# Performance work log

Measured on AMD Instinct MI355X. Metric: run time of the kernel, lower is better.

The kernel has to match this reference:

```python
import jax, jax.numpy as jnp
from jax import lax
import numpy as np

NUM_HEAD = 12
EPS = 1e-5            # torch LayerNorm default
NEG_INF = 1.0e12      # self.inf_value in the source
LEAKY_SLOPE = 0.01    # torch LeakyReLU default
MASK_FIRST = True     # maskedAtten=True applies only to block 0


def _layer_norm(x, s, b):
    m = jnp.mean(x, axis=-1, keepdims=True)
    v = jnp.var(x, axis=-1, keepdims=True)
    return (x - m) / jnp.sqrt(v + EPS) * s + b


def _forward(x, conv_w, conv_b, pos, ln0_s, ln0_b, Wq, bq, Wk, bk, Wv, bv,
             Wo, bo, ln1_s, ln1_b, W1, b1, W2, b2, proj_w, proj_b):
    B, C, H, W = x.shape
    E = conv_w.shape[0]
    P = conv_w.shape[-1]
    hd = E // NUM_HEAD

    # patch embed: Conv2d(C, E, P, stride=P)
    h = lax.conv_general_dilated(x, conv_w, (P, P), 'VALID',
                                 dimension_numbers=('NCHW', 'OIHW', 'NCHW'))
    h = h + conv_b[None, :, None, None]
    L = h.shape[2] * h.shape[3]
    h = h.reshape(B, E, L).transpose(0, 2, 1) + pos  # (B, L, E)

    causal = jnp.triu(jnp.ones((L, L), dtype=bool), 1)
    n_layers = Wq.shape[0]
    for i in range(n_layers):
        # --- attention block ---
        xn = _layer_norm(h, ln0_s[i], ln0_b[i])
        q = (xn @ Wq[i] + bq[i]).reshape(B, L, NUM_HEAD, hd).transpose(0, 2, 1, 3)
        k = (xn @ Wk[i] + bk[i]).reshape(B, L, NUM_HEAD, hd).transpose(0, 2, 1, 3)
        v = (xn @ Wv[i] + bv[i]).reshape(B, L, NUM_HEAD, hd).transpose(0, 2, 1, 3)
        scores = jnp.einsum('bhqd,bhkd->bhqk', q, k) * (hd ** -0.5)
        if i == 0 and MASK_FIRST:
            scores = jnp.where(causal, -NEG_INF, scores)
        a = jax.nn.softmax(scores, axis=-1)
        o = jnp.einsum('bhqk,bhkd->bhqd', a, v)  # (B, NH, L, hd)
        # faithful to torch source: reshape(bs, l, emb) WITHOUT permuting heads back
        o = o.reshape(B, L, E)
        o = o @ Wo[i] + bo[i]
        h = o + h  # residual onto pre-LN input
        # --- MLP block ---
        xr = _layer_norm(h, ln1_s[i], ln1_b[i])
        m = xr @ W1[i] + b1[i]
        m = jnp.where(m >= 0, m, LEAKY_SLOPE * m)
        m = m @ W2[i] + b2[i]
        h = m + xr  # residual onto post-LN (as in source)

    y = h @ proj_w + proj_b               # (B, L, C*P*P)
    y = y.transpose(0, 2, 1).reshape(B, C, H, W)
    return y


def setup_inputs() -> dict:
    key = jax.random.key(0)
    B, C, H, W = 8, 3, 384, 384
    P, E, NL = 16, 768, 8
    FF = 4 * E
    L = (H // P) * (W // P)  # 576
    CPP = C * P * P          # 768
    s = 0.02
    ks = jax.random.split(key, 24)
    f32 = jnp.float32
    inp = {
        'x': jax.random.normal(ks[0], (B, C, H, W), f32),
        'conv_w': jax.random.normal(ks[1], (E, C, P, P), f32) * s,
        'conv_b': jax.random.normal(ks[2], (E,), f32) * s,
        'pos': jax.random.normal(ks[3], (1, L, E), f32),
        'ln0_s': jnp.ones((NL, E), f32),
        'ln0_b': jnp.zeros((NL, E), f32),
        'Wq': jax.random.normal(ks[4], (NL, E, E), f32) * s,
        'bq': jax.random.normal(ks[5], (NL, E), f32) * s,
        'Wk': jax.random.normal(ks[6], (NL, E, E), f32) * s,
        'bk': jax.random.normal(ks[7], (NL, E), f32) * s,
        'Wv': jax.random.normal(ks[8], (NL, E, E), f32) * s,
        'bv': jax.random.normal(ks[9], (NL, E), f32) * s,
        'Wo': jax.random.normal(ks[10], (NL, E, E), f32) * s,
        'bo': jax.random.normal(ks[11], (NL, E), f32) * s,
        'ln1_s': jnp.ones((NL, E), f32),
        'ln1_b': jnp.zeros((NL, E), f32),
        'W1': jax.random.normal(ks[12], (NL, E, FF), f32) * s,
        'b1': jax.random.normal(ks[13], (NL, FF), f32) * s,
        'W2': jax.random.normal(ks[14], (NL, FF, E), f32) * s,
        'b2': jax.random.normal(ks[15], (NL, E), f32) * s,
        'proj_w': jax.random.normal(ks[16], (E, CPP), f32) * s,
        'proj_b': jax.random.normal(ks[17], (CPP,), f32) * s,
    }
    return inp


def reference(x, conv_w, conv_b, pos, ln0_s, ln0_b, Wq, bq, Wk, bk, Wv, bv,
              Wo, bo, ln1_s, ln1_b, W1, b1, W2, b2, proj_w, proj_b):
    return _forward(x, conv_w, conv_b, pos, ln0_s, ln0_b, Wq, bq, Wk, bk,
                    Wv, bv, Wo, bo, ln1_s, ln1_b, W1, b1, W2, b2,
                    proj_w, proj_b)
```

## Files before the change

kernel.cpp:

```cpp
#include <hip/hip_runtime.h>
#include <hip/hip_bf16.h>
#include <stdint.h>

#define NLAYERS 8
#define LSEQ 576
#define EMB 768
#define NHEAD 12
#define HDIM 64
#define FFDIM 3072
#define BLROWS 4608

typedef __attribute__((ext_vector_type(8))) short short8;
typedef __attribute__((ext_vector_type(4))) float floatx4;

__device__ __forceinline__ float b2f(short s) {
    union { float f; uint32_t u; } x; x.u = ((uint32_t)(uint16_t)s) << 16; return x.f;
}
__device__ __forceinline__ short f2b(float f) {
    union { float f; uint32_t u; } x; x.f = f;
    uint32_t r = x.u + 0x7fffu + ((x.u >> 16) & 1u);
    return (short)(r >> 16);
}

#define GLDS16(gp, lp) __builtin_amdgcn_global_load_lds( \
    (const __attribute__((address_space(1))) void*)(gp), \
    (__attribute__((address_space(3))) void*)(lp), 16, 0, 0)

__device__ __forceinline__ void xcd_remap(int& bx, int& by) {
    const int gx = gridDim.x;
    const int n  = gx * gridDim.y;
    const int orig = by * gx + bx;
    const int q = n >> 3, r = n & 7;
    const int xcd = orig & 7;
    const int wgid = (xcd < r ? xcd * (q + 1) : r * (q + 1) + (xcd - r) * q) + (orig >> 3);
    bx = wgid % gx;
    by = wgid / gx;
}

template<int DEPTH, int RES, bool ADD_POS, bool LEAKY, int OUTM, bool QKV>
__global__ __launch_bounds__(256)
void gemm_bt(const short* __restrict__ A, const short* __restrict__ Bt,
             const float* __restrict__ bias, const float* __restrict__ pos,
             const void* __restrict__ res, void* __restrict__ Cout,
             short* __restrict__ aux_kp, short* __restrict__ aux_vt,
             int N, int K)
{
    __shared__ short As[DEPTH * 64 * 64];
    __shared__ short Bs[DEPTH * 128 * 64];
    int bx = blockIdx.x, by = blockIdx.y;
    xcd_remap(bx, by);
    const int t    = threadIdx.x;
    const int lane = t & 63;
    const int w    = t >> 6;
    const int m0   = by * 64;
    const int n0   = bx * 128;
    const int wm   = (w >> 1) * 32;
    const int wn   = (w & 1) * 64;

    floatx4 acc[2][4];
#pragma unroll
    for (int i = 0; i < 2; ++i)
#pragma unroll
        for (int j = 0; j < 4; ++j)
            acc[i][j] = (floatx4){0.f, 0.f, 0.f, 0.f};

    const int srow = t >> 3;
    const int sch  = t & 7;
    const short* Ag = A  + (size_t)m0 * K;
    const short* Bg = Bt + (size_t)n0 * K;
    const int nt = K >> 6;

#define STAGE(buf, k0)                                                              \
    {                                                                               \
        _Pragma("unroll")                                                           \
        for (int i = 0; i < 2; ++i) {                                               \
            int row = srow + i * 32;                                                \
            GLDS16(Ag + (size_t)row * K + (k0) + ((sch ^ (row & 7)) << 3),          \
                   &As[(buf) * 4096 + (size_t)(t + i * 256) * 8]);                  \
        }                                                                           \
        _Pragma("unroll")                                                           \
        for (int i = 0; i < 4; ++i) {                                               \
            int row = srow + i * 32;                                                \
            GLDS16(Bg + (size_t)row * K + (k0) + ((sch ^ (row & 7)) << 3),          \
                   &Bs[(buf) * 8192 + (size_t)(t + i * 256) * 8]);                  \
        }                                                                           \
    }

#define COMPUTE(buf)                                                                \
    {                                                                               \
        _Pragma("unroll")                                                           \
        for (int ks = 0; ks < 2; ++ks) {                                            \
            short8 af[2], bf[4];                                                    \
            _Pragma("unroll")                                                       \
            for (int i = 0; i < 2; ++i) {                                           \
                int row = wm + i * 16 + (lane & 15);                                \
                int ch  = (ks * 4 + (lane >> 4)) ^ (row & 7);                       \
                af[i] = *(const short8*)&As[(buf) * 4096 + row * 64 + ch * 8];      \
            }                                                                       \
            _Pragma("unroll")                                                       \
            for (int j = 0; j < 4; ++j) {                                           \
                int row = wn + j * 16 + (lane & 15);                                \
                int ch  = (ks * 4 + (lane >> 4)) ^ (row & 7);                       \
                bf[j] = *(const short8*)&Bs[(buf) * 8192 + row * 64 + ch * 8];      \
            }                                                                       \
            _Pragma("unroll")                                                       \
            for (int i = 0; i < 2; ++i)                                             \
                _Pragma("unroll")                                                   \
                for (int j = 0; j < 4; ++j)                                         \
                    acc[i][j] = __builtin_amdgcn_mfma_f32_16x16x32_bf16(            \
                        af[i], bf[j], acc[i][j], 0, 0, 0);                          \
        }                                                                           \
    }

    if constexpr (DEPTH == 2) {
        STAGE(0, 0);
        __syncthreads();
        int cur = 0;
        for (int k0 = 0; k0 < K; k0 += 64) {
            if (k0 + 64 < K) STAGE(cur ^ 1, k0 + 64);
            COMPUTE(cur);
            __syncthreads();
            cur ^= 1;
        }
    } else {
        STAGE(0, 0);
        STAGE(1, 64);
        asm volatile("s_waitcnt vmcnt(6)" ::: "memory");
        __builtin_amdgcn_sched_barrier(0);
        __builtin_amdgcn_s_barrier();
        int cur = 0, stg = 2;
        for (int tt = 0; tt < nt; ++tt) {
            if (tt + 2 < nt) STAGE(stg, (tt + 2) << 6);
            COMPUTE(cur);
            if (tt + 1 < nt) {
                if (tt + 2 < nt) { asm volatile("s_waitcnt vmcnt(6)" ::: "memory"); }
                else             { asm volatile("s_waitcnt vmcnt(0)" ::: "memory"); }
                __builtin_amdgcn_sched_barrier(0);
                __builtin_amdgcn_s_barrier();
                __builtin_amdgcn_sched_barrier(0);
            }
            cur = (cur + 1 == DEPTH) ? 0 : cur + 1;
            stg = (stg + 1 == DEPTH) ? 0 : stg + 1;
        }
    }
#undef STAGE
#undef COMPUTE

    const int colb = n0 + wn + (lane & 15);
    const int rowb = m0 + wm + ((lane >> 4) * 4);
#pragma unroll
    for (int i = 0; i < 2; ++i) {
#pragma unroll
        for (int j = 0; j < 4; ++j) {
            const int col = colb + j * 16;
            const float bv = bias[col];
#pragma unroll
            for (int r = 0; r < 4; ++r) {
                const int row = rowb + i * 16 + r;
                float v = acc[i][j][r] + bv;
                if constexpr (ADD_POS) v += pos[(size_t)(row % LSEQ) * N + col];
                if constexpr (RES == 1) v += ((const float*)res)[(size_t)row * N + col];
                if constexpr (RES == 2) v += b2f(((const short*)res)[(size_t)row * N + col]);
                if constexpr (LEAKY)   v = v >= 0.f ? v : 0.01f * v;
                if constexpr (QKV) {
                    const int b = row / LSEQ, l = row % LSEQ;
                    const short sv16 = f2b(v);
                    if (col < 768) {
                        ((short*)Cout)[(size_t)row * 768 + col] = sv16;
                    } else if (col < 1536) {
                        const int d = col - 768, hh = d >> 6, dd = d & 63;
                        const size_t bh = (size_t)b * 12 + hh;
                        aux_kp[(bh * LSEQ + l) * 64 + (dd & 7) + (((dd >> 3) ^ (l & 7)) << 3)] = sv16;
                    } else {
                        const int d = col - 1536, hh = d >> 6, dd = d & 63;
                        const size_t bh = (size_t)b * 12 + hh;
                        aux_vt[(bh * 64 + dd) * LSEQ + (l & ~63) + ((l & 63) ^ ((dd & 7) << 3))] = sv16;
                    }
                } else if constexpr (OUTM == 1) {
                    ((float*)Cout)[(size_t)row * N + col] = v;
                } else if constexpr (OUTM == 2) {
                    ((float*)Cout)[(size_t)row * N + col] = v;
                    aux_kp[(size_t)row * N + col] = f2b(v);
                } else {
                    ((short*)Cout)[(size_t)row * N + col] = f2b(v);
                }
            }
        }
    }
}

__global__ __launch_bounds__(256)
void ln_kernel(const float* __restrict__ h, const float* __restrict__ g,
               const float* __restrict__ bbias, short* __restrict__ outb)
{
    const int row = blockIdx.x;
    const float* x = h + (size_t)row * EMB;
    const int t = threadIdx.x;
    float v0 = x[t], v1 = x[t + 256], v2 = x[t + 512];
    float s  = v0 + v1 + v2;
    float ss = v0 * v0 + v1 * v1 + v2 * v2;
#pragma unroll
    for (int m = 1; m < 64; m <<= 1) {
        s  += __shfl_xor(s, m, 64);
        ss += __shfl_xor(ss, m, 64);
    }
    __shared__ float red[8];
    if ((t & 63) == 0) { red[t >> 6] = s; red[4 + (t >> 6)] = ss; }
    __syncthreads();
    float S  = red[0] + red[1] + red[2] + red[3];
    float SS = red[4] + red[5] + red[6] + red[7];
    float mean = S * (1.f / 768.f);
    float var  = SS * (1.f / 768.f) - mean * mean;
    float rstd = rsqrtf(var + 1e-5f);
    const size_t base = (size_t)row * EMB;
#pragma unroll
    for (int q = 0; q < 3; ++q) {
        int e = t + q * 256;
        float v = (q == 0 ? v0 : (q == 1 ? v1 : v2));
        float y = (v - mean) * rstd * g[e] + bbias[e];
        outb[base + e] = f2b(y);
    }
}

__global__ __launch_bounds__(256)
void attn_mfma(const short* __restrict__ qbuf, const short* __restrict__ kp,
               const short* __restrict__ vt, short* __restrict__ oout, int causal)
{
    const int qt = blockIdx.x, bh = blockIdx.y;
    const int b = bh / 12, h = bh % 12;
    const int t = threadIdx.x, lane = t & 63, w = t >> 6;

    __shared__ short Ks[64 * 64];
    __shared__ short Vs[64 * 64];
    __shared__ short Plds[4][16][72];

    const int nrow = lane & 15;
    const int kch  = (lane >> 4) * 8;
    const int swz  = (lane & 7) << 3;

    short8 aq[2];
    {
        const short* qrow = qbuf + ((size_t)(b * LSEQ) + qt * 64 + w * 16 + nrow) * 768 + h * 64 + kch;
        aq[0] = *(const short8*)qrow;
        aq[1] = *(const short8*)(qrow + 32);
    }

    float m[4], lsum[4];
    floatx4 oacc[4];
#pragma unroll
    for (int r = 0; r < 4; ++r) { m[r] = -3e38f; lsum[r] = 0.f; }
#pragma unroll
    for (int j = 0; j < 4; ++j) oacc[j] = (floatx4){0.f, 0.f, 0.f, 0.f};

    const int ktend = causal ? qt : 8;
    const short* ksrc = kp + ((size_t)bh * LSEQ) * 64;
    const short* vsrc = vt + ((size_t)bh * 64) * LSEQ;

    for (int kt = 0; kt <= ktend; ++kt) {
        __syncthreads();
        {
            const short* kt_src = ksrc + (size_t)(kt * 64) * 64;
            GLDS16(kt_src + (size_t)t * 8,          &Ks[(size_t)t * 8]);
            GLDS16(kt_src + (size_t)(t + 256) * 8,  &Ks[(size_t)(t + 256) * 8]);
            int f0 = t, f1 = t + 256;
            GLDS16(vsrc + (size_t)(f0 >> 3) * LSEQ + kt * 64 + (f0 & 7) * 8, &Vs[(size_t)f0 * 8]);
            GLDS16(vsrc + (size_t)(f1 >> 3) * LSEQ + kt * 64 + (f1 & 7) * 8, &Vs[(size_t)f1 * 8]);
        }
        __syncthreads();

        floatx4 sc[4];
#pragma unroll
        for (int j = 0; j < 4; ++j) sc[j] = (floatx4){0.f, 0.f, 0.f, 0.f};
#pragma unroll
        for (int s = 0; s < 2; ++s) {
#pragma unroll
            for (int j = 0; j < 4; ++j) {
                short8 bk = *(const short8*)&Ks[(16 * j + nrow) * 64 + ((kch + 32 * s) ^ swz)];
                sc[j] = __builtin_amdgcn_mfma_f32_16x16x32_bf16(aq[s], bk, sc[j], 0, 0, 0);
            }
        }
        float sv[4][4];
#pragma unroll
        for (int j = 0; j < 4; ++j)
#pragma unroll
            for (int r = 0; r < 4; ++r) {
                float v = sc[j][r] * 0.125f;
                if (causal && kt == qt) {
                    int key = kt * 64 + 16 * j + nrow;
                    int qr  = qt * 64 + w * 16 + (lane >> 4) * 4 + r;
                    if (key > qr) v = -1e12f;
                }
                sv[j][r] = v;
            }
#pragma unroll
        for (int r = 0; r < 4; ++r) {
            float tm = fmaxf(fmaxf(sv[0][r], sv[1][r]), fmaxf(sv[2][r], sv[3][r]));
            tm = fmaxf(tm, __shfl_xor(tm, 1, 64));
            tm = fmaxf(tm, __shfl_xor(tm, 2, 64));
            tm = fmaxf(tm, __shfl_xor(tm, 4, 64));
            tm = fmaxf(tm, __shfl_xor(tm, 8, 64));
            float nm = fmaxf(m[r], tm);
            float c  = __expf(m[r] - nm);
            m[r] = nm;
            float ps = 0.f;
#pragma unroll
            for (int j = 0; j < 4; ++j) {
                float p = __expf(sv[j][r] - nm);
                sv[j][r] = p;
                ps += p;
            }
            lsum[r] = lsum[r] * c + ps;
#pragma unroll
            for (int j = 0; j < 4; ++j) oacc[j][r] *= c;
        }
#pragma unroll
        for (int j = 0; j < 4; ++j)
#pragma unroll
            for (int r = 0; r < 4; ++r)
                Plds[w][(lane >> 4) * 4 + r][16 * j + nrow] = f2b(sv[j][r]);
        short8 ap[2];
#pragma unroll
        for (int s = 0; s < 2; ++s)
            ap[s] = *(const short8*)&Plds[w][nrow][kch + 32 * s];
#pragma unroll
        for (int s = 0; s < 2; ++s) {
#pragma unroll
            for (int j = 0; j < 4; ++j) {
                short8 bv = *(const short8*)&Vs[(16 * j + nrow) * 64 + ((kch + 32 * s) ^ swz)];
                oacc[j] = __builtin_amdgcn_mfma_f32_16x16x32_bf16(ap[s], bv, oacc[j], 0, 0, 0);
            }
        }
    }

    float inv[4];
#pragma unroll
    for (int r = 0; r < 4; ++r) {
        float L = lsum[r];
        L += __shfl_xor(L, 1, 64);
        L += __shfl_xor(L, 2, 64);
        L += __shfl_xor(L, 4, 64);
        L += __shfl_xor(L, 8, 64);
        inv[r] = 1.f / L;
    }
#pragma unroll
    for (int j = 0; j < 4; ++j)
#pragma unroll
        for (int r = 0; r < 4; ++r) {
            size_t lq = (size_t)qt * 64 + w * 16 + (lane >> 4) * 4 + r;
            oout[((size_t)bh * LSEQ + lq) * 64 + 16 * j + nrow] = f2b(oacc[j][r] * inv[r]);
        }
}

__global__ void transpose_f2b(const float* __restrict__ in, short* __restrict__ out,
                              int R, int C, long long ibs, long long obs)
{
    __shared__ float tile[32][33];
    const int b = blockIdx.z;
    const float* inb = in + (long long)b * ibs;
    short* outb = out + (long long)b * obs;
    const int r0 = blockIdx.y * 32, c0 = blockIdx.x * 32;
    const int tx = threadIdx.x, ty = threadIdx.y;
#pragma unroll
    for (int i = 0; i < 32; i += 8) tile[ty + i][tx] = inb[(size_t)(r0 + ty + i) * C + c0 + tx];
    __syncthreads();
#pragma unroll
    for (int i = 0; i < 32; i += 8) outb[(size_t)(c0 + ty + i) * R + r0 + tx] = f2b(tile[tx][ty + i]);
}

__global__ void transpose_f2f(const float* __restrict__ in, float* __restrict__ out,
                              int R, int C, long long ibs, long long obs)
{
    __shared__ float tile[32][33];
    const int b = blockIdx.z;
    const float* inb = in + (long long)b * ibs;
    float* outb = out + (long long)b * obs;
    const int r0 = blockIdx.y * 32, c0 = blockIdx.x * 32;
    const int tx = threadIdx.x, ty = threadIdx.y;
#pragma unroll
    for (int i = 0; i < 32; i += 8) tile[ty + i][tx] = inb[(size_t)(r0 + ty + i) * C + c0 + tx];
    __syncthreads();
#pragma unroll
    for (int i = 0; i < 32; i += 8) outb[(size_t)(c0 + ty + i) * R + r0 + tx] = tile[tx][ty + i];
}

__global__ void concat_qkv_bias(const float* __restrict__ bq, const float* __restrict__ bk,
                                const float* __restrict__ bv, float* __restrict__ out)
{
    int i = blockIdx.x * 256 + threadIdx.x;
    int layer = i / 2304, j = i % 2304;
    float v;
    if (j < 768)       v = bq[layer * 768 + j];
    else if (j < 1536) v = bk[layer * 768 + j - 768];
    else               v = bv[layer * 768 + j - 1536];
    out[i] = v;
}

__global__ void im2col_kernel(const float* __restrict__ x, short* __restrict__ xcol)
{
    const size_t idx = (size_t)blockIdx.x * 256 + threadIdx.x;
    const int k = (int)(idx % 768);
    const size_t m = idx / 768;
    const int c  = k >> 8;
    const int ky = (k >> 4) & 15;
    const int kx = k & 15;
    const int b  = (int)(m / 576);
    const int l  = (int)(m % 576);
    const int ph = l / 24, pw = l % 24;
    xcol[idx] = f2b(x[((size_t)(b * 3 + c) * 384 + ph * 16 + ky) * 384 + pw * 16 + kx]);
}

__global__ void cast_f32_b16(const float* __restrict__ in, short* __restrict__ out, int n)
{
    int i = blockIdx.x * 256 + threadIdx.x;
    if (i < n) out[i] = f2b(in[i]);
}

extern "C" void kernel_launch(void* const* d_in, const int* in_sizes, int n_in,
                              void* d_out, int out_size, void* d_ws, size_t ws_size,
                              hipStream_t stream)
{
    const float* x      = (const float*)d_in[0];
    const float* conv_w = (const float*)d_in[1];
    const float* conv_b = (const float*)d_in[2];
    const float* pos    = (const float*)d_in[3];
    const float* ln0_s  = (const float*)d_in[4];
    const float* ln0_b  = (const float*)d_in[5];
    const float* Wq     = (const float*)d_in[6];
    const float* bq     = (const float*)d_in[7];
    const float* Wk     = (const float*)d_in[8];
    const float* bk     = (const float*)d_in[9];
    const float* Wv     = (const float*)d_in[10];
    const float* bv     = (const float*)d_in[11];
    const float* Wo     = (const float*)d_in[12];
    const float* bo     = (const float*)d_in[13];
    const float* ln1_s  = (const float*)d_in[14];
    const float* ln1_b  = (const float*)d_in[15];
    const float* W1     = (const float*)d_in[16];
    const float* b1     = (const float*)d_in[17];
    const float* W2     = (const float*)d_in[18];
    const float* b2     = (const float*)d_in[19];
    const float* proj_w = (const float*)d_in[20];
    const float* proj_b = (const float*)d_in[21];

    char* ws = (char*)d_ws;
    short* qkvT  = (short*)(ws);
    short* woT   = (short*)(ws + 28311552);
    short* w1T   = (short*)(ws + 37748736);
    short* w2T   = (short*)(ws + 75497472);
    short* projT = (short*)(ws + 113246208);
    float* qkvb  = (float*)(ws + 114425856);
    short* tmpA  = (short*)(ws + 114499584);
    float* h     = (float*)(ws + 142811136);
    short* xn    = (short*)(ws + 156966912);
    short* xrb   = (short*)(ws + 164044800);
    short* qbuf  = (short*)(ws + 185278464);
    short* o     = (short*)(ws + 206512128);
    short* convB = (short*)(ws + 213590016);

    short* kp = tmpA;
    short* vt = tmpA + 3538944;

    dim3 tb(32, 8);
    transpose_f2b<<<dim3(24, 24, 8), tb, 0, stream>>>(Wq, qkvT,           768, 768, 589824, 1769472);
    transpose_f2b<<<dim3(24, 24, 8), tb, 0, stream>>>(Wk, qkvT + 589824,  768, 768, 589824, 1769472);
    transpose_f2b<<<dim3(24, 24, 8), tb, 0, stream>>>(Wv, qkvT + 1179648, 768, 768, 589824, 1769472);
    transpose_f2b<<<dim3(24, 24, 8), tb, 0, stream>>>(Wo, woT,            768, 768, 589824, 589824);
    transpose_f2b<<<dim3(96, 24, 8), tb, 0, stream>>>(W1, w1T,            768, 3072, 2359296, 2359296);
    transpose_f2b<<<dim3(24, 96, 8), tb, 0, stream>>>(W2, w2T,            3072, 768, 2359296, 2359296);
    transpose_f2b<<<dim3(24, 24, 1), tb, 0, stream>>>(proj_w, projT,      768, 768, 0, 0);
    cast_f32_b16<<<2304, 256, 0, stream>>>(conv_w, convB, 589824);
    concat_qkv_bias<<<72, 256, 0, stream>>>(bq, bk, bv, qkvb);

    im2col_kernel<<<13824, 256, 0, stream>>>(x, tmpA);
    gemm_bt<3, 0, true, false, 1, false><<<dim3(6, 72), 256, 0, stream>>>(
        tmpA, convB, conv_b, pos, nullptr, h, nullptr, nullptr, 768, 768);

    for (int i = 0; i < NLAYERS; ++i) {
        ln_kernel<<<4608, 256, 0, stream>>>(h, ln0_s + i * 768, ln0_b + i * 768, xn);
        gemm_bt<2, 0, false, false, 0, true><<<dim3(18, 72), 256, 0, stream>>>(
            xn, qkvT + (size_t)i * 1769472, qkvb + i * 2304, nullptr, nullptr, qbuf, kp, vt, 2304, 768);
        attn_mfma<<<dim3(9, 96), 256, 0, stream>>>(qbuf, kp, vt, o, i == 0 ? 1 : 0);
        gemm_bt<3, 1, false, false, 1, false><<<dim3(6, 72), 256, 0, stream>>>(
            o, woT + (size_t)i * 589824, bo + i * 768, nullptr, h, h, nullptr, nullptr, 768, 768);
        ln_kernel<<<4608, 256, 0, stream>>>(h, ln1_s + i * 768, ln1_b + i * 768, xrb);
        gemm_bt<2, 0, false, true, 0, false><<<dim3(24, 72), 256, 0, stream>>>(
            xrb, w1T + (size_t)i * 2359296, b1 + i * 3072, nullptr, nullptr, tmpA, nullptr, nullptr, 3072, 768);
        if (i < NLAYERS - 1) {
            gemm_bt<3, 2, false, false, 1, false><<<dim3(6, 72), 256, 0, stream>>>(
                tmpA, w2T + (size_t)i * 2359296, b2 + i * 768, nullptr, xrb, h, nullptr, nullptr, 768, 3072);
        } else {
            gemm_bt<3, 2, false, false, 2, false><<<dim3(6, 72), 256, 0, stream>>>(
                tmpA, w2T + (size_t)i * 2359296, b2 + i * 768, nullptr, xrb, h, xn, nullptr, 768, 3072);
        }
    }

    short* hb = xn;
    float* yf = (float*)tmpA;
    gemm_bt<3, 0, false, false, 1, false><<<dim3(6, 72), 256, 0, stream>>>(
        hb, projT, proj_b, nullptr, nullptr, yf, nullptr, nullptr, 768, 768);
    transpose_f2f<<<dim3(24, 18, 8), tb, 0, stream>>>(yf, (float*)d_out, 576, 768, 442368, 442368);
}
```

Baseline: 1.620 ms.

## Split-K the N=768 GEMMs into two halves with a separate combine kernel

The GEMMs with N=768 (patch embed, out-projection, MLP down-projection, final projection) previously launched only 432 workgroups. They now split K across two z-slices, giving 864 workgroups. Each slice writes fp32 partials to its own buffer, and a new elementwise combine kernel adds the partials, bias, pos and residual, plus an optional bf16 copy. This is meant to fill the GPU's compute units better on these small-N GEMMs. The cost is an extra fp32 partial round-trip through memory and one more kernel launch per GEMM.

Result: slower. 1.780 ms (+9.9%).

```diff
diff --git a/kernel.cpp b/kernel.cpp
--- a/kernel.cpp
+++ b/kernel.cpp
@@ -11,6 +11,7 @@
 #define BLROWS 4608
 
 typedef __attribute__((ext_vector_type(8))) short short8;
+typedef __attribute__((ext_vector_type(4))) short short4v;
 typedef __attribute__((ext_vector_type(4))) float floatx4;
 
 __device__ __forceinline__ float b2f(short s) {
@@ -37,7 +38,7 @@
     by = wgid / gx;
 }
 
-template<int DEPTH, int RES, bool ADD_POS, bool LEAKY, int OUTM, bool QKV>
+template<int DEPTH, int RES, bool ADD_POS, bool LEAKY, int OUTM, bool QKV, bool SPLITK>
 __global__ __launch_bounds__(256)
 void gemm_bt(const short* __restrict__ A, const short* __restrict__ Bt,
              const float* __restrict__ bias, const float* __restrict__ pos,
@@ -57,6 +58,9 @@
     const int wm   = (w >> 1) * 32;
     const int wn   = (w & 1) * 64;
 
+    const int klen  = SPLITK ? (K >> 1) : K;
+    const int kbase = SPLITK ? blockIdx.z * klen : 0;
+
     floatx4 acc[2][4];
 #pragma unroll
     for (int i = 0; i < 2; ++i)
@@ -66,9 +70,9 @@
 
     const int srow = t >> 3;
     const int sch  = t & 7;
-    const short* Ag = A  + (size_t)m0 * K;
-    const short* Bg = Bt + (size_t)n0 * K;
-    const int nt = K >> 6;
+    const short* Ag = A  + (size_t)m0 * K + kbase;
+    const short* Bg = Bt + (size_t)n0 * K + kbase;
+    const int nt = klen >> 6;
 
 #define STAGE(buf, k0)                                                              \
     {                                                                               \
@@ -116,8 +120,8 @@
         STAGE(0, 0);
         __syncthreads();
         int cur = 0;
-        for (int k0 = 0; k0 < K; k0 += 64) {
-            if (k0 + 64 < K) STAGE(cur ^ 1, k0 + 64);
+        for (int k0 = 0; k0 < klen; k0 += 64) {
+            if (k0 + 64 < klen) STAGE(cur ^ 1, k0 + 64);
             COMPUTE(cur);
             __syncthreads();
             cur ^= 1;
@@ -148,6 +152,19 @@
 
     const int colb = n0 + wn + (lane & 15);
     const int rowb = m0 + wm + ((lane >> 4) * 4);
+
+    if constexpr (SPLITK) {
+        float* P = blockIdx.z ? (float*)aux_kp : (float*)Cout;
+#pragma unroll
+        for (int i = 0; i < 2; ++i)
+#pragma unroll
+            for (int j = 0; j < 4; ++j)
+#pragma unroll
+                for (int r = 0; r < 4; ++r)
+                    P[(size_t)(rowb + i * 16 + r) * N + colb + j * 16] = acc[i][j][r];
+        return;
+    }
+
 #pragma unroll
     for (int i = 0; i < 2; ++i) {
 #pragma unroll
@@ -189,6 +206,46 @@
     }
 }
 
+template<int RES, bool ADD_POS, int OUTM>
+__global__ __launch_bounds__(256)
+void combinek(const float* __restrict__ P0, const float* __restrict__ P1,
+              const float* __restrict__ bias, const float* __restrict__ pos,
+              const void* __restrict__ res, float* __restrict__ out,
+              short* __restrict__ auxb)
+{
+    const size_t i4 = ((size_t)blockIdx.x * 256 + threadIdx.x) * 4;
+    const int row = (int)(i4 / 768);
+    const int col = (int)(i4 % 768);
+    floatx4 a = *(const floatx4*)&P0[i4];
+    floatx4 b = *(const floatx4*)&P1[i4];
+    floatx4 bv = *(const floatx4*)&bias[col];
+    floatx4 v;
+#pragma unroll
+    for (int j = 0; j < 4; ++j) v[j] = a[j] + b[j] + bv[j];
+    if constexpr (ADD_POS) {
+        floatx4 p = *(const floatx4*)&pos[(size_t)(row % LSEQ) * 768 + col];
+#pragma unroll
+        for (int j = 0; j < 4; ++j) v[j] += p[j];
+    }
+    if constexpr (RES == 1) {
+        floatx4 rr = *(const floatx4*)&((const float*)res)[i4];
+#pragma unroll
+        for (int j = 0; j < 4; ++j) v[j] += rr[j];
+    }
+    if constexpr (RES == 2) {
+        short4v rr = *(const short4v*)&((const short*)res)[i4];
+#pragma unroll
+        for (int j = 0; j < 4; ++j) v[j] += b2f(rr[j]);
+    }
+    *(floatx4*)&out[i4] = v;
+    if constexpr (OUTM == 2) {
+        short4v ob;
+#pragma unroll
+        for (int j = 0; j < 4; ++j) ob[j] = f2b(v[j]);
+        *(short4v*)&auxb[i4] = ob;
+    }
+}
+
 __global__ __launch_bounds__(256)
 void ln_kernel(const float* __restrict__ h, const float* __restrict__ g,
                const float* __restrict__ bbias, short* __restrict__ outb)
@@ -459,6 +516,8 @@
 
     short* kp = tmpA;
     short* vt = tmpA + 3538944;
+    float* P1 = (float*)qbuf;
+    float* tmpAF = (float*)tmpA;
 
     dim3 tb(32, 8);
     transpose_f2b<<<dim3(24, 24, 8), tb, 0, stream>>>(Wq, qkvT,           768, 768, 589824, 1769472);
@@ -472,31 +531,34 @@
     concat_qkv_bias<<<72, 256, 0, stream>>>(bq, bk, bv, qkvb);
 
     im2col_kernel<<<13824, 256, 0, stream>>>(x, tmpA);
-    gemm_bt<3, 0, true, false, 1, false><<<dim3(6, 72), 256, 0, stream>>>(
-        tmpA, convB, conv_b, pos, nullptr, h, nullptr, nullptr, 768, 768);
+    gemm_bt<3, 0, false, false, 1, false, true><<<dim3(6, 72, 2), 256, 0, stream>>>(
+        tmpA, convB, nullptr, nullptr, nullptr, h, (short*)P1, nullptr, 768, 768);
+    combinek<0, true, 1><<<3456, 256, 0, stream>>>(h, P1, conv_b, pos, nullptr, h, nullptr);
 
     for (int i = 0; i < NLAYERS; ++i) {
         ln_kernel<<<4608, 256, 0, stream>>>(h, ln0_s + i * 768, ln0_b + i * 768, xn);
-        gemm_bt<2, 0, false, false, 0, true><<<dim3(18, 72), 256, 0, stream>>>(
+        gemm_bt<2, 0, false, false, 0, true, false><<<dim3(18, 72), 256, 0, stream>>>(
             xn, qkvT + (size_t)i * 1769472, qkvb + i * 2304, nullptr, nullptr, qbuf, kp, vt, 2304, 768);
         attn_mfma<<<dim3(9, 96), 256, 0, stream>>>(qbuf, kp, vt, o, i == 0 ? 1 : 0);
-        gemm_bt<3, 1, false, false, 1, false><<<dim3(6, 72), 256, 0, stream>>>(
-            o, woT + (size_t)i * 589824, bo + i * 768, nullptr, h, h, nullptr, nullptr, 768, 768);
+        gemm_bt<3, 0, false, false, 1, false, true><<<dim3(6, 72, 2), 256, 0, stream>>>(
+            o, woT + (size_t)i * 589824, nullptr, nullptr, nullptr, tmpAF, (short*)P1, nullptr, 768, 768);
+        combinek<1, false, 1><<<3456, 256, 0, stream>>>(tmpAF, P1, bo + i * 768, nullptr, h, h, nullptr);
         ln_kernel<<<4608, 256, 0, stream>>>(h, ln1_s + i * 768, ln1_b + i * 768, xrb);
-        gemm_bt<2, 0, false, true, 0, false><<<dim3(24, 72), 256, 0, stream>>>(
+        gemm_bt<2, 0, false, true, 0, false, false><<<dim3(24, 72), 256, 0, stream>>>(
             xrb, w1T + (size_t)i * 2359296, b1 + i * 3072, nullptr, nullptr, tmpA, nullptr, nullptr, 3072, 768);
+        gemm_bt<3, 0, false, false, 1, false, true><<<dim3(6, 72, 2), 256, 0, stream>>>(
+            tmpA, w2T + (size_t)i * 2359296, nullptr, nullptr, nullptr, h, (short*)P1, nullptr, 768, 3072);
         if (i < NLAYERS - 1) {
-            gemm_bt<3, 2, false, false, 1, false><<<dim3(6, 72), 256, 0, stream>>>(
-                tmpA, w2T + (size_t)i * 2359296, b2 + i * 768, nullptr, xrb, h, nullptr, nullptr, 768, 3072);
+            combinek<2, false, 1><<<3456, 256, 0, stream>>>(h, P1, b2 + i * 768, nullptr, xrb, h, nullptr);
         } else {
-            gemm_bt<3, 2, false, false, 2, false><<<dim3(6, 72), 256, 0, stream>>>(
-                tmpA, w2T + (size_t)i * 2359296, b2 + i * 768, nullptr, xrb, h, xn, nullptr, 768, 3072);
+            combinek<2, false, 2><<<3456, 256, 0, stream>>>(h, P1, b2 + i * 768, nullptr, xrb, h, xn);
         }
     }
 
     short* hb = xn;
-    float* yf = (float*)tmpA;
-    gemm_bt<3, 0, false, false, 1, false><<<dim3(6, 72), 256, 0, stream>>>(
-        hb, projT, proj_b, nullptr, nullptr, yf, nullptr, nullptr, 768, 768);
+    float* yf = tmpAF;
+    gemm_bt<3, 0, false, false, 1, false, true><<<dim3(6, 72, 2), 256, 0, stream>>>(
+        hb, projT, nullptr, nullptr, nullptr, h, (short*)P1, nullptr, 768, 768);
+    combinek<0, false, 1><<<3456, 256, 0, stream>>>(h, P1, proj_b, nullptr, nullptr, yf, nullptr);
     transpose_f2f<<<dim3(24, 18, 8), tb, 0, stream>>>(yf, (float*)d_out, 576, 768, 442368, 442368);
 }
```

## Double-buffer K/V tiles in attention kernel and raise MFMA wave priority

Applied to the files above, without the earlier changes.

Splits the shared-memory K and V tiles into two buffers, so the next tile's direct-to-LDS global loads are issued before computing on the current tile. Each iteration then needs one barrier instead of two. The MFMA sections are also wrapped in s_setprio to favour matrix issue. This hides global-load latency behind compute, at the cost of doubling K/V LDS use, which may lower occupancy. Attention is only part of the total runtime, so the end-to-end effect is limited.

Measured after the change: 1.648 ms. About the same (+1.7%).

```diff
diff --git a/kernel.cpp b/kernel.cpp
--- a/kernel.cpp
+++ b/kernel.cpp
@@ -230,8 +230,8 @@
     const int b = bh / 12, h = bh % 12;
     const int t = threadIdx.x, lane = t & 63, w = t >> 6;
 
-    __shared__ short Ks[64 * 64];
-    __shared__ short Vs[64 * 64];
+    __shared__ short Ks[2][64 * 64];
+    __shared__ short Vs[2][64 * 64];
     __shared__ short Plds[4][16][72];
 
     const int nrow = lane & 15;
@@ -256,29 +256,39 @@
     const short* ksrc = kp + ((size_t)bh * LSEQ) * 64;
     const short* vsrc = vt + ((size_t)bh * 64) * LSEQ;
 
+#define STAGE_KV(buf, kt)                                                             \
+    {                                                                                 \
+        const short* kt_src = ksrc + (size_t)((kt) * 64) * 64;                        \
+        GLDS16(kt_src + (size_t)t * 8,         &Ks[buf][(size_t)t * 8]);              \
+        GLDS16(kt_src + (size_t)(t + 256) * 8, &Ks[buf][(size_t)(t + 256) * 8]);      \
+        GLDS16(vsrc + (size_t)(t >> 3) * LSEQ + (kt) * 64 + (t & 7) * 8,              \
+               &Vs[buf][(size_t)t * 8]);                                              \
+        GLDS16(vsrc + (size_t)((t + 256) >> 3) * LSEQ + (kt) * 64 + (t & 7) * 8,      \
+               &Vs[buf][(size_t)(t + 256) * 8]);                                      \
+    }
+
+    STAGE_KV(0, 0);
+    asm volatile("s_waitcnt vmcnt(0)" ::: "memory");
+    __builtin_amdgcn_sched_barrier(0);
+    __builtin_amdgcn_s_barrier();
+
     for (int kt = 0; kt <= ktend; ++kt) {
-        __syncthreads();
-        {
-            const short* kt_src = ksrc + (size_t)(kt * 64) * 64;
-            GLDS16(kt_src + (size_t)t * 8,          &Ks[(size_t)t * 8]);
-            GLDS16(kt_src + (size_t)(t + 256) * 8,  &Ks[(size_t)(t + 256) * 8]);
-            int f0 = t, f1 = t + 256;
-            GLDS16(vsrc + (size_t)(f0 >> 3) * LSEQ + kt * 64 + (f0 & 7) * 8, &Vs[(size_t)f0 * 8]);
-            GLDS16(vsrc + (size_t)(f1 >> 3) * LSEQ + kt * 64 + (f1 & 7) * 8, &Vs[(size_t)f1 * 8]);
-        }
-        __syncthreads();
+        const int cur = kt & 1;
+        if (kt < ktend) STAGE_KV(cur ^ 1, kt + 1);
 
         floatx4 sc[4];
 #pragma unroll
         for (int j = 0; j < 4; ++j) sc[j] = (floatx4){0.f, 0.f, 0.f, 0.f};
+        __builtin_amdgcn_s_setprio(1);
 #pragma unroll
         for (int s = 0; s < 2; ++s) {
 #pragma unroll
             for (int j = 0; j < 4; ++j) {
-                short8 bk = *(const short8*)&Ks[(16 * j + nrow) * 64 + ((kch + 32 * s) ^ swz)];
+                short8 bk = *(const short8*)&Ks[cur][(16 * j + nrow) * 64 + ((kch + 32 * s) ^ swz)];
                 sc[j] = __builtin_amdgcn_mfma_f32_16x16x32_bf16(aq[s], bk, sc[j], 0, 0, 0);
             }
         }
+        __builtin_amdgcn_s_setprio(0);
         float sv[4][4];
 #pragma unroll
         for (int j = 0; j < 4; ++j)
@@ -322,15 +332,23 @@
 #pragma unroll
         for (int s = 0; s < 2; ++s)
             ap[s] = *(const short8*)&Plds[w][nrow][kch + 32 * s];
+        __builtin_amdgcn_s_setprio(1);
 #pragma unroll
         for (int s = 0; s < 2; ++s) {
 #pragma unroll
             for (int j = 0; j < 4; ++j) {
-                short8 bv = *(const short8*)&Vs[(16 * j + nrow) * 64 + ((kch + 32 * s) ^ swz)];
+                short8 bv = *(const short8*)&Vs[cur][(16 * j + nrow) * 64 + ((kch + 32 * s) ^ swz)];
                 oacc[j] = __builtin_amdgcn_mfma_f32_16x16x32_bf16(ap[s], bv, oacc[j], 0, 0, 0);
             }
         }
-    }
+        __builtin_amdgcn_s_setprio(0);
+        if (kt < ktend) {
+            asm volatile("s_waitcnt vmcnt(0)" ::: "memory");
+            __builtin_amdgcn_sched_barrier(0);
+            __builtin_amdgcn_s_barrier();
+        }
+    }
+#undef STAGE_KV
 
     float inv[4];
 #pragma unroll
```
